# Kernel tuning notes

Hardware: AMD Instinct MI355X
Metric: run time of the kernel (lower is better)

## Reference

```python
import jax, jax.numpy as jnp
import numpy as np

B, S, E = 2, 2048, 2048
N_HEAD = 16
HEAD_DIM = E // N_HEAD  # 128
MP_NUM = 4              # hardcoded in the torch forward
ROTARY_DIM = 64


def setup_inputs() -> dict:
    key = jax.random.key(0)
    k1, k2, k3 = jax.random.split(key, 3)
    return {
        "hidden_states": jax.random.normal(k1, (B, S, E), jnp.float32) * 0.02,
        "w_qkv": jax.random.normal(k2, (3 * E, E), jnp.float32) * 0.02,  # torch Linear weight [out,in]
        "w_out": jax.random.normal(k3, (E, E), jnp.float32) * 0.02,
    }


def _rotate_every_two(x):
    # (..., d) -> interleaved (-x2, x1) as in GPT-J/CodeGen
    x1 = x[..., 0::2]
    x2 = x[..., 1::2]
    return jnp.stack((-x2, x1), axis=-1).reshape(x.shape)


def reference(hidden_states, w_qkv, w_out):
    b, s, e = hidden_states.shape
    local = e // MP_NUM  # per-mp-shard channel count

    # qkv projection (no bias), then mp_num split: order is (query, value, key)
    qkv = jnp.einsum("bse,fe->bsf", hidden_states, w_qkv)  # [B,S,3E]
    qkv = qkv.reshape(b, s, MP_NUM, 3 * local)
    q = qkv[..., :local].reshape(b, s, N_HEAD, HEAD_DIM)
    v = qkv[..., local:2 * local].reshape(b, s, N_HEAD, HEAD_DIM)
    k = qkv[..., 2 * local:].reshape(b, s, N_HEAD, HEAD_DIM)

    # partial rotary (rotate-every-two) on first ROTARY_DIM channels
    inv_freq = 1.0 / (10000.0 ** (jnp.arange(0, ROTARY_DIM, 2, dtype=jnp.float32) / ROTARY_DIM))
    freqs = jnp.arange(s, dtype=jnp.float32)[:, None] * inv_freq[None, :]  # [S, R/2]
    sin = jnp.repeat(jnp.sin(freqs), 2, axis=-1)[None, :, None, :]  # [1,S,1,R]
    cos = jnp.repeat(jnp.cos(freqs), 2, axis=-1)[None, :, None, :]

    def rope(x):
        x_rot = x[..., :ROTARY_DIM]
        x_pass = x[..., ROTARY_DIM:]
        x_rot = x_rot * cos + _rotate_every_two(x_rot) * sin
        return jnp.concatenate([x_rot, x_pass], axis=-1)

    q = rope(q)
    k = rope(k)

    # [B,S,H,D] -> [B,H,S,D]
    q = q.transpose(0, 2, 1, 3)
    k = k.transpose(0, 2, 1, 3)
    v = v.transpose(0, 2, 1, 3)

    scale = jnp.sqrt(jnp.asarray(HEAD_DIM, dtype=q.dtype))
    scores = jnp.einsum("bhqd,bhkd->bhqk", q, k) / scale  # [B,H,S,S]
    causal = jnp.tril(jnp.ones((s, s), dtype=bool))
    scores = jnp.where(causal[None, None, :, :], scores, jnp.finfo(scores.dtype).min)
    attn = jax.nn.softmax(scores, axis=-1)

    out = jnp.einsum("bhqk,bhkd->bhqd", attn, v)  # [B,H,S,D]
    out = out.transpose(0, 2, 1, 3).reshape(b, s, e)  # merge heads
    return jnp.einsum("bse,fe->bsf", out, w_out)  # out_proj (no bias)
```

## Files before the change

kernel.cpp:

```cpp
#include <hip/hip_runtime.h>

typedef unsigned short u16;
typedef unsigned int u32;
typedef __attribute__((ext_vector_type(4))) float f32x4;
typedef __attribute__((ext_vector_type(8))) short s16x8;

#define DEVI static __device__ __forceinline__


DEVI u16 f2bf(float f) {
  u32 u = __float_as_uint(f);
  return (u16)((u + 0x7FFFu + ((u >> 16) & 1u)) >> 16);
}
DEVI float bf2f(u16 h) { return __uint_as_float(((u32)h) << 16); }

DEVI void async_copy16(const u16* g, u16* l) {
  __builtin_amdgcn_global_load_lds((__attribute__((address_space(1))) void*)g,
                                   (__attribute__((address_space(3))) void*)l, 16, 0, 0);
}

__global__ __launch_bounds__(256) void cast_bf16_kernel(const float* __restrict__ src,
                                                        u16* __restrict__ dst, int n4) {
  int i = blockIdx.x * 256 + threadIdx.x;
  if (i < n4) {
    const float4 v = ((const float4*)src)[i];
    ushort4 o;
    o.x = f2bf(v.x); o.y = f2bf(v.y); o.z = f2bf(v.z); o.w = f2bf(v.w);
    ((ushort4*)dst)[i] = o;
  }
}

template <int EPI>
__global__ __launch_bounds__(256, 2) void gemm_bt_kernel(
    const u16* __restrict__ A, const u16* __restrict__ Bm, int K, int N,
    float* __restrict__ C, u16* __restrict__ qo, u16* __restrict__ ko, u16* __restrict__ vo) {
  __shared__ __attribute__((aligned(16))) u16 As[128 * 32];
  __shared__ __attribute__((aligned(16))) u16 Bs[128 * 32];
  const int tid = threadIdx.x;
  const int w = tid >> 6, lane = tid & 63;
  const int quad = lane >> 4, l16 = lane & 15;
  const int wrow = (w >> 1) * 64, wcol = (w & 1) * 64;
  const long tileM = (long)blockIdx.y * 128;
  const long tileN = (long)blockIdx.x * 128;

  f32x4 acc[4][4];
#pragma unroll
  for (int i = 0; i < 4; ++i)
#pragma unroll
    for (int j = 0; j < 4; ++j) acc[i][j] = f32x4{0.f, 0.f, 0.f, 0.f};

  const int ldr = lane >> 2;
  const int ldc = (lane & 3) * 8;

  for (int k0 = 0; k0 < K; k0 += 32) {
    __syncthreads();
#pragma unroll
    for (int c = 0; c < 2; ++c) {
      const int r0 = (w * 2 + c) * 16;
      async_copy16(A + (tileM + r0 + ldr) * (long)K + (k0 + ldc), As + r0 * 32);
      async_copy16(Bm + (tileN + r0 + ldr) * (long)K + (k0 + ldc), Bs + r0 * 32);
    }
    __builtin_amdgcn_s_waitcnt(0x0f70);
    __syncthreads();

    s16x8 af[4], bfr[4];
#pragma unroll
    for (int i = 0; i < 4; ++i)
      af[i] = *(const s16x8*)(As + (wrow + i * 16 + l16) * 32 + quad * 8);
#pragma unroll
    for (int j = 0; j < 4; ++j)
      bfr[j] = *(const s16x8*)(Bs + (wcol + j * 16 + l16) * 32 + quad * 8);
#pragma unroll
    for (int i = 0; i < 4; ++i)
#pragma unroll
      for (int j = 0; j < 4; ++j)
        acc[i][j] = __builtin_amdgcn_mfma_f32_16x16x32_bf16(af[i], bfr[j], acc[i][j], 0, 0, 0);
  }

#pragma unroll
  for (int i = 0; i < 4; ++i) {
#pragma unroll
    for (int j = 0; j < 4; ++j) {
#pragma unroll
      for (int r = 0; r < 4; ++r) {
        const long row = tileM + wrow + i * 16 + quad * 4 + r;
        const long col = tileN + wcol + j * 16 + l16;
        const float v = acc[i][j][r];
        if (EPI == 0) {
          C[row * N + col] = v;
        } else {
          const int b = (int)(row >> 11), s = (int)(row & 2047);
          const int cl = (int)col;
          const int mp = cl / 1536;
          const int cc = cl - mp * 1536;
          const int part = cc >> 9;
          const int idx = cc & 511;
          const int head = mp * 4 + (idx >> 7);
          const int dim = idx & 127;
          const long bh = b * 16 + head;
          const u16 bv = f2bf(v);
          if (part == 0)      qo[(bh * 2048 + s) * 128 + dim] = bv;
          else if (part == 2) ko[(bh * 2048 + s) * 128 + dim] = bv;
          else                vo[(bh * 128 + dim) * 2048 + s] = bv;
        }
      }
    }
  }
}

__global__ __launch_bounds__(256) void rope_kernel(u16* __restrict__ q, u16* __restrict__ k) {
  const int tid = threadIdx.x;
  const long row = (long)blockIdx.x * 4 + (tid >> 6);
  const int p = tid & 63;
  const int s = (int)(row & 2047);
  u16* base = (blockIdx.y == 0 ? q : k) + row * 128 + p * 2;
  const float scale = (blockIdx.y == 0) ? 0.12751743f : 1.0f;
  const float x0 = bf2f(base[0]), x1 = bf2f(base[1]);
  float y0, y1;
  if (p < 32) {
    const float inv = exp2f((float)p * (-13.287712379549449f / 32.0f));
    const float fr = (float)s * inv;
    const float sn = sinf(fr), cs = cosf(fr);
    y0 = (x0 * cs - x1 * sn) * scale;
    y1 = (x1 * cs + x0 * sn) * scale;
  } else {
    y0 = x0 * scale;
    y1 = x1 * scale;
  }
  base[0] = f2bf(y0);
  base[1] = f2bf(y1);
}

__global__ __launch_bounds__(256, 2) void attn_kernel(
    const u16* __restrict__ q, const u16* __restrict__ k,
    const u16* __restrict__ vT, u16* __restrict__ out) {
  __shared__ __attribute__((aligned(16))) u16 Ks[2][64 * 128];
  __shared__ __attribute__((aligned(16))) u16 Vs[2][128 * 64];
  __shared__ __attribute__((aligned(16))) u16 Ps[4][16 * 88];
  const int tid = threadIdx.x;
  const int w = tid >> 6, lane = tid & 63;
  const int quad = lane >> 4, l16 = lane & 15;
  const int qt = 31 - (blockIdx.x >> 5);
  const int bh = blockIdx.x & 31;
  const int qbase = qt * 64 + w * 16;

  const u16* qp = q + ((long)bh * 2048 + qbase) * 128;
  const u16* kp = k + (long)bh * 2048 * 128;
  const u16* vp = vT + (long)bh * 128 * 2048;

  s16x8 qf[4];
#pragma unroll
  for (int c = 0; c < 4; ++c)
    qf[c] = *(const s16x8*)(qp + l16 * 128 + c * 32 + quad * 8);

  f32x4 acc[8];
#pragma unroll
  for (int d = 0; d < 8; ++d) acc[d] = f32x4{0.f, 0.f, 0.f, 0.f};
  float mrun[4], lrun[4];
#pragma unroll
  for (int r = 0; r < 4; ++r) { mrun[r] = -1e30f; lrun[r] = 0.f; }

  auto stage = [&](int k0, int buf) {
    const int ko = lane >> 4, cl = lane & 15;
#pragma unroll
    for (int i = 0; i < 4; ++i) {
      const int keyt = w * 16 + i * 4;
      const int key = keyt + ko;
      async_copy16(kp + (long)(k0 + key) * 128 + ((cl ^ (key & 15)) << 3),
                   &Ks[buf][keyt * 128]);
    }
    const int ld = lane >> 3, c8 = lane & 7;
#pragma unroll
    for (int i = 0; i < 4; ++i) {
      const int db = w * 32 + i * 8;
      const int d = db + ld;
      async_copy16(vp + (long)d * 2048 + k0 + ((c8 ^ (d & 7)) << 3),
                   &Vs[buf][db * 64]);
    }
  };

  stage(0, 0);

  for (int t = 0; t <= qt; ++t) {
    const int k0 = t * 64;
    const u16* Ksc = Ks[t & 1];
    const u16* Vsc = Vs[t & 1];
    __builtin_amdgcn_s_waitcnt(0x0f70);
    __syncthreads();
    if (t < qt) stage(k0 + 64, (t + 1) & 1);

    f32x4 sc[4];
#pragma unroll
    for (int g = 0; g < 4; ++g) {
      sc[g] = f32x4{0.f, 0.f, 0.f, 0.f};
#pragma unroll
      for (int c = 0; c < 4; ++c) {
        const s16x8 kf = *(const s16x8*)(
            &Ksc[(g * 16 + l16) * 128 + ((((c << 2) + quad) ^ l16) << 3)]);
        sc[g] = __builtin_amdgcn_mfma_f32_16x16x32_bf16(qf[c], kf, sc[g], 0, 0, 0);
      }
    }
    if (t == qt) {
#pragma unroll
      for (int g = 0; g < 4; ++g) {
        const int col = k0 + g * 16 + l16;
#pragma unroll
        for (int r = 0; r < 4; ++r)
          if (col > qbase + quad * 4 + r) sc[g][r] = -1e30f;
      }
    }
    float p[4][4], alpha[4];
#pragma unroll
    for (int r = 0; r < 4; ++r) {
      float mx = fmaxf(fmaxf(sc[0][r], sc[1][r]), fmaxf(sc[2][r], sc[3][r]));
#pragma unroll
      for (int off = 1; off < 16; off <<= 1) mx = fmaxf(mx, __shfl_xor(mx, off, 64));
      const float mnew = fmaxf(mrun[r], mx);
      alpha[r] = exp2f(mrun[r] - mnew);
      mrun[r] = mnew;
      float sm = 0.f;
#pragma unroll
      for (int g = 0; g < 4; ++g) { p[g][r] = exp2f(sc[g][r] - mnew); sm += p[g][r]; }
#pragma unroll
      for (int off = 1; off < 16; off <<= 1) sm += __shfl_xor(sm, off, 64);
      lrun[r] = lrun[r] * alpha[r] + sm;
    }
#pragma unroll
    for (int d = 0; d < 8; ++d)
#pragma unroll
      for (int r = 0; r < 4; ++r) acc[d][r] *= alpha[r];
#pragma unroll
    for (int r = 0; r < 4; ++r)
#pragma unroll
      for (int g = 0; g < 4; ++g)
        Ps[w][(quad * 4 + r) * 88 + g * 16 + l16] = f2bf(p[g][r]);
    __builtin_amdgcn_s_waitcnt(0xc07f);
#pragma unroll
    for (int kk = 0; kk < 2; ++kk) {
      const s16x8 pf = *(const s16x8*)(&Ps[w][l16 * 88 + kk * 32 + quad * 8]);
#pragma unroll
      for (int dd = 0; dd < 8; ++dd) {
        const s16x8 vf = *(const s16x8*)(
            &Vsc[(dd * 16 + l16) * 64 + ((((kk << 2) + quad) ^ (l16 & 7)) << 3)]);
        acc[dd] = __builtin_amdgcn_mfma_f32_16x16x32_bf16(pf, vf, acc[dd], 0, 0, 0);
      }
    }
  }

  const int b = bh >> 4, h = bh & 15;
  u16* op = out + ((long)b * 2048 + qbase) * 2048 + h * 128;
#pragma unroll
  for (int d = 0; d < 8; ++d)
#pragma unroll
    for (int r = 0; r < 4; ++r) {
      const float v = acc[d][r] / lrun[r];
      op[(long)(quad * 4 + r) * 2048 + d * 16 + l16] = f2bf(v);
    }
}

extern "C" void kernel_launch(void* const* d_in, const int* in_sizes, int n_in,
                              void* d_out, int out_size, void* d_ws, size_t ws_size,
                              hipStream_t stream) {
  const float* hidden = (const float*)d_in[0];
  const float* w_qkv = (const float*)d_in[1];
  const float* w_out = (const float*)d_in[2];
  float* out = (float*)d_out;
  char* ws = (char*)d_ws;

  u16* hid_b  = (u16*)(ws + (size_t)0);
  u16* wqkv_b = (u16*)(ws + (size_t)16777216);
  u16* wout_b = (u16*)(ws + (size_t)41943040);
  u16* qb     = (u16*)(ws + (size_t)50331648);
  u16* kb     = (u16*)(ws + (size_t)67108864);
  u16* vb     = (u16*)(ws + (size_t)83886080);
  u16* ao     = (u16*)(ws + (size_t)100663296);

  cast_bf16_kernel<<<8192, 256, 0, stream>>>(hidden, hid_b, 2097152);
  cast_bf16_kernel<<<12288, 256, 0, stream>>>(w_qkv, wqkv_b, 3145728);
  cast_bf16_kernel<<<4096, 256, 0, stream>>>(w_out, wout_b, 1048576);

  gemm_bt_kernel<1><<<dim3(48, 32), 256, 0, stream>>>(hid_b, wqkv_b, 2048, 6144,
                                                      nullptr, qb, kb, vb);
  rope_kernel<<<dim3(16384, 2), 256, 0, stream>>>(qb, kb);
  attn_kernel<<<1024, 256, 0, stream>>>(qb, kb, vb, ao);
  gemm_bt_kernel<0><<<dim3(16, 32), 256, 0, stream>>>(ao, wout_b, 2048, 2048,
                                                      out, nullptr, nullptr, nullptr);
}
```

Baseline: 446.0 us.

## Double-buffer GEMM LDS loads with XOR swizzle and fuse cast kernels

The GEMM main loop now uses two LDS buffers, so the async global-to-LDS copy of the next K-slice is issued while MFMAs run on the current slice. This removes one barrier per iteration. The LDS column layout is XOR-swizzled by row to reduce bank conflicts on the fragment reads. The three fp32-to-bf16 cast launches are merged into one kernel to cut launch overhead. Doubling LDS use may lower occupancy relative to the two-blocks-per-CU launch bound.

```diff
diff --git a/kernel.cpp b/kernel.cpp
--- a/kernel.cpp
+++ b/kernel.cpp
@@ -19,23 +19,34 @@
                                    (__attribute__((address_space(3))) void*)l, 16, 0, 0);
 }
 
-__global__ __launch_bounds__(256) void cast_bf16_kernel(const float* __restrict__ src,
-                                                        u16* __restrict__ dst, int n4) {
+__global__ __launch_bounds__(256) void cast3_kernel(
+    const float* __restrict__ s0, u16* __restrict__ d0, int n0,
+    const float* __restrict__ s1, u16* __restrict__ d1, int n1,
+    const float* __restrict__ s2, u16* __restrict__ d2, int n2) {
   int i = blockIdx.x * 256 + threadIdx.x;
-  if (i < n4) {
-    const float4 v = ((const float4*)src)[i];
-    ushort4 o;
-    o.x = f2bf(v.x); o.y = f2bf(v.y); o.z = f2bf(v.z); o.w = f2bf(v.w);
-    ((ushort4*)dst)[i] = o;
-  }
+  const float* s;
+  u16* d;
+  if (i < n0) {
+    s = s0; d = d0;
+  } else if (i < n0 + n1) {
+    s = s1; d = d1; i -= n0;
+  } else if (i < n0 + n1 + n2) {
+    s = s2; d = d2; i -= n0 + n1;
+  } else {
+    return;
+  }
+  const float4 v = ((const float4*)s)[i];
+  ushort4 o;
+  o.x = f2bf(v.x); o.y = f2bf(v.y); o.z = f2bf(v.z); o.w = f2bf(v.w);
+  ((ushort4*)d)[i] = o;
 }
 
 template <int EPI>
 __global__ __launch_bounds__(256, 2) void gemm_bt_kernel(
     const u16* __restrict__ A, const u16* __restrict__ Bm, int K, int N,
     float* __restrict__ C, u16* __restrict__ qo, u16* __restrict__ ko, u16* __restrict__ vo) {
-  __shared__ __attribute__((aligned(16))) u16 As[128 * 32];
-  __shared__ __attribute__((aligned(16))) u16 Bs[128 * 32];
+  __shared__ __attribute__((aligned(16))) u16 As[2][128 * 32];
+  __shared__ __attribute__((aligned(16))) u16 Bs[2][128 * 32];
   const int tid = threadIdx.x;
   const int w = tid >> 6, lane = tid & 63;
   const int quad = lane >> 4, l16 = lane & 15;
@@ -49,32 +60,50 @@
 #pragma unroll
     for (int j = 0; j < 4; ++j) acc[i][j] = f32x4{0.f, 0.f, 0.f, 0.f};
 
-  const int ldr = lane >> 2;
-  const int ldc = (lane & 3) * 8;
-
+  const u16* aptr[2];
+  const u16* bptr[2];
+  int ldso[2];
+#pragma unroll
+  for (int c = 0; c < 2; ++c) {
+    const int r0 = (w * 2 + c) * 16;
+    const int row = r0 + (lane >> 2);
+    const int colsw = (((lane & 3) ^ ((row >> 1) & 3)) << 3);
+    aptr[c] = A + (tileM + row) * (long)K + colsw;
+    bptr[c] = Bm + (tileN + row) * (long)K + colsw;
+    ldso[c] = r0 * 32;
+  }
+
+  auto stage = [&](int k0, int buf) {
+#pragma unroll
+    for (int c = 0; c < 2; ++c) {
+      async_copy16(aptr[c] + k0, &As[buf][ldso[c]]);
+      async_copy16(bptr[c] + k0, &Bs[buf][ldso[c]]);
+    }
+  };
+
+  stage(0, 0);
+
+  const int psw = (quad ^ ((l16 >> 1) & 3)) << 3;
+
+  int buf = 0;
   for (int k0 = 0; k0 < K; k0 += 32) {
-    __syncthreads();
-#pragma unroll
-    for (int c = 0; c < 2; ++c) {
-      const int r0 = (w * 2 + c) * 16;
-      async_copy16(A + (tileM + r0 + ldr) * (long)K + (k0 + ldc), As + r0 * 32);
-      async_copy16(Bm + (tileN + r0 + ldr) * (long)K + (k0 + ldc), Bs + r0 * 32);
-    }
     __builtin_amdgcn_s_waitcnt(0x0f70);
     __syncthreads();
+    if (k0 + 32 < K) stage(k0 + 32, buf ^ 1);
 
     s16x8 af[4], bfr[4];
 #pragma unroll
     for (int i = 0; i < 4; ++i)
-      af[i] = *(const s16x8*)(As + (wrow + i * 16 + l16) * 32 + quad * 8);
+      af[i] = *(const s16x8*)(&As[buf][(wrow + i * 16 + l16) * 32 + psw]);
 #pragma unroll
     for (int j = 0; j < 4; ++j)
-      bfr[j] = *(const s16x8*)(Bs + (wcol + j * 16 + l16) * 32 + quad * 8);
+      bfr[j] = *(const s16x8*)(&Bs[buf][(wcol + j * 16 + l16) * 32 + psw]);
 #pragma unroll
     for (int i = 0; i < 4; ++i)
 #pragma unroll
       for (int j = 0; j < 4; ++j)
         acc[i][j] = __builtin_amdgcn_mfma_f32_16x16x32_bf16(af[i], bfr[j], acc[i][j], 0, 0, 0);
+    buf ^= 1;
   }
 
 #pragma unroll
@@ -275,9 +304,9 @@
   u16* vb     = (u16*)(ws + (size_t)83886080);
   u16* ao     = (u16*)(ws + (size_t)100663296);
 
-  cast_bf16_kernel<<<8192, 256, 0, stream>>>(hidden, hid_b, 2097152);
-  cast_bf16_kernel<<<12288, 256, 0, stream>>>(w_qkv, wqkv_b, 3145728);
-  cast_bf16_kernel<<<4096, 256, 0, stream>>>(w_out, wout_b, 1048576);
+  cast3_kernel<<<24576, 256, 0, stream>>>(hidden, hid_b, 2097152,
+                                          w_qkv, wqkv_b, 3145728,
+                                          w_out, wout_b, 1048576);
 
   gemm_bt_kernel<1><<<dim3(48, 32), 256, 0, stream>>>(hid_b, wqkv_b, 2048, 6144,
                                                       nullptr, qb, kb, vb);
```

After: 438.5 us. About the same (-1.7%).
